# Kernel optimization log

Measured on AMD Instinct MI355X. Metric: run time of the kernel, lower is better.

## Reference

```python
import jax, jax.numpy as jnp
from jax import lax
import numpy as np

KERNEL = 3
DILATION = 2
STRIDE = 2
MU = 0.1


def mask_dial(kernel_size, dilation, mu):
    # Faithful numpy port of CustomConv.mask_dial (constant fuzzy mask).
    d = dilation - 1
    mid = [0.0] * d
    lim = d // 2 if d % 2 == 0 else d // 2 + 1
    diff = (1.0 - mu) / lim
    for i in range(lim):
        mid[i] = 1.0 - (i + 1) * diff
        mid[d - 1 - i] = 1.0 - (i + 1) * diff
    filter1 = []
    for i in range(2 * kernel_size - 1):
        filter1 = filter1 + ([0.0] if i % 2 == 0 else mid)
    filter2 = [[0.0 for _ in range(d + 2)] for _ in range(d)]
    for i in range(lim):
        for j in range(i + 2):
            filter2[i][j] = mid[i]
            filter2[i][d + 1 - j] = mid[i]
            filter2[d - i - 1][j] = mid[i]
            filter2[d - i - 1][d + 1 - j] = mid[i]
        for j in range(i + 1, lim):
            filter2[i][j + 1] = mid[j]
            filter2[i][d - j] = mid[j]
            filter2[d - i - 1][j + 1] = mid[j]
            filter2[d - i - 1][d - j] = mid[j]
    filter3 = [x[1:] for x in filter2]
    for i in range(kernel_size - 2):
        for j in range(len(filter2)):
            filter2[j] = filter2[j] + filter3[j]
    result = []
    for i in range(2 * kernel_size - 1):
        result = result + ([filter1] if i % 2 == 0 else filter2)
    m = np.array(result, dtype=np.float32)
    m[m == 1.0] = 0.0  # self.fuz[self.fuz == 1] = 0
    return m

# constant (kk, kk) mask, kk = dilation*(kernel-1)+1 = 5
FUZ_MASK = jnp.asarray(mask_dial(KERNEL, DILATION, MU))


def setup_inputs() -> dict:
    key = jax.random.key(0)
    k1, k2, k3 = jax.random.split(key, 3)
    B, Cin, H, W = 16, 128, 112, 112
    Cout = 256
    stdv = float(np.sqrt(6.0 / (Cin * KERNEL ** 2 + Cout * KERNEL ** 2)))
    input_ = jax.random.normal(k1, (B, Cin, H, W), dtype=jnp.float32)
    weight = jax.random.uniform(k2, (Cout, Cin, KERNEL, KERNEL), minval=-stdv, maxval=stdv, dtype=jnp.float32)
    bias1 = jax.random.uniform(k3, (Cout,), minval=-stdv, maxval=stdv, dtype=jnp.float32)
    return {"input_": input_, "weight": weight, "bias1": bias1}


def reference(input_, weight, bias1):
    Cout, Cin = weight.shape[0], weight.shape[1]
    dn = ("NCHW", "OIHW", "NCHW")
    # term 1: standard dilated conv (im2col with kernel=3, dilation=2 in original)
    out_w = lax.conv_general_dilated(
        input_, weight, window_strides=(STRIDE, STRIDE), padding="VALID",
        rhs_dilation=(DILATION, DILATION), dimension_numbers=dn)
    # term 2: fuzzy conv: kernel = fuz_mask * bias1[o], dense 5x5, dilation 1
    kk = FUZ_MASK.shape[0]
    fuz_kernel = bias1[:, None, None, None] * jnp.broadcast_to(
        FUZ_MASK.astype(input_.dtype), (Cout, Cin, kk, kk))
    out_f = lax.conv_general_dilated(
        input_, fuz_kernel, window_strides=(STRIDE, STRIDE), padding="VALID",
        dimension_numbers=dn)
    return out_w + out_f
```

## Files before the change

kernel.cpp:

```cpp
#include <hip/hip_runtime.h>
#include <hip/hip_bf16.h>

typedef __bf16 bf16x8 __attribute__((ext_vector_type(8)));
typedef float f32x4 __attribute__((ext_vector_type(4)));
typedef unsigned short u16x8 __attribute__((ext_vector_type(8)));

#define B_    16
#define CIN   128
#define H_    112
#define W_    112
#define COUT  256
#define HO    54
#define WO    54
#define M_PER_B (HO*WO)
#define HW    (H_*W_)

__device__ __forceinline__ unsigned short f2bf(float v) {
    __hip_bfloat16 h = __float2bfloat16(v);
    return __builtin_bit_cast(unsigned short, h);
}

__global__ __launch_bounds__(256) void sum_kernel(
    const float* __restrict__ in, const float* __restrict__ w,
    float* __restrict__ S, unsigned short* __restrict__ Wf)
{
    const int blk = blockIdx.x;
    const int tid = threadIdx.x;
    if (blk < B_ * H_) {
        __shared__ f32x4 red[8][28];
        const int b = blk / H_, h = blk % H_;
        if (tid < 224) {
            const int cg = tid / 28, ws = tid % 28;
            const float* p = in + ((size_t)(b * CIN + cg * 16) * H_ + h) * W_ + 4 * ws;
            f32x4 acc = (f32x4){0.f, 0.f, 0.f, 0.f};
            #pragma unroll
            for (int k = 0; k < 16; ++k)
                acc += *reinterpret_cast<const f32x4*>(p + (size_t)k * HW);
            red[cg][ws] = acc;
        }
        __syncthreads();
        if (tid < 28) {
            f32x4 s = red[0][tid];
            #pragma unroll
            for (int g = 1; g < 8; ++g) s += red[g][tid];
            *reinterpret_cast<f32x4*>(S + (size_t)(b * H_ + h) * W_ + 4 * tid) = s;
        }
    } else {
        int cid = (blk - B_ * H_) * 256 + tid;
        if (cid < 9 * 4 * 16 * 64) {
            int L   = cid & 63;
            int g   = (cid >> 6) & 15;
            int c0  = (cid >> 10) & 3;
            int t   = cid >> 12;
            int o   = g * 16 + (L & 15);
            int cb  = c0 * 32 + (L >> 4) * 8;
            u16x8 v;
            #pragma unroll
            for (int e = 0; e < 8; ++e)
                v[e] = f2bf(w[(size_t)(o * CIN + cb + e) * 9 + t]);
            *reinterpret_cast<u16x8*>(Wf + (size_t)cid * 8) = v;
        }
    }
}

__global__ __launch_bounds__(128) void t_kernel(
    const float* __restrict__ S, float* __restrict__ T)
{
    __shared__ float Sr[5][112];
    const int blk = blockIdx.x;
    const int tid = threadIdx.x;
    const int b = blk / HO, y = blk % HO;
    for (int task = tid; task < 5 * 28; task += 128) {
        int row = task / 28, w4 = task % 28;
        *reinterpret_cast<f32x4*>(&Sr[row][4 * w4]) =
            *reinterpret_cast<const f32x4*>(S + (size_t)(b * H_ + 2 * y + row) * W_ + 4 * w4);
    }
    __syncthreads();
    if (tid < WO) {
        int x = tid;
        float s25 = 0.f, s9 = 0.f;
        #pragma unroll
        for (int i = 0; i < 5; ++i) {
            #pragma unroll
            for (int j = 0; j < 5; ++j) {
                float v = Sr[i][2 * x + j];
                s25 += v;
                if (!(i & 1) && !(j & 1)) s9 += v;
            }
        }
        T[(size_t)b * M_PER_B + y * WO + x] = 0.1f * (s25 - s9);
    }
}

__global__ __launch_bounds__(256, 3) void conv_kernel(
    const float* __restrict__ in, const unsigned short* __restrict__ Wf,
    const float* __restrict__ T, const float* __restrict__ bias1,
    float* __restrict__ out)
{
    __shared__ unsigned short patch[168 * 128];

    const int tid = threadIdx.x;
    int bid = blockIdx.x;
    int wg  = (bid & 7) * 108 + (bid >> 3);
    const int b = wg / HO;
    const int y = wg % HO;

    const float* inb = in + (size_t)b * CIN * HW;
    #pragma unroll
    for (int it = 0; it < 42; ++it) {
        int ch = tid + it * 256;
        int ws = ch % 28;
        int cr = ch / 28;
        int r  = cr % 3;
        int c  = cr / 3;
        f32x4 v = *reinterpret_cast<const f32x4*>(
            inb + ((size_t)c * H_ + (2 * y + 2 * r)) * W_ + 4 * ws);
        int p0 = r * 56 + 2 * ws;
        patch[p0 * 128 + (c ^ ((p0 & 7) << 3))] = f2bf(v[0]);
        int p1 = p0 + 1;
        patch[p1 * 128 + (c ^ ((p1 & 7) << 3))] = f2bf(v[2]);
    }
    __syncthreads();

    const int lane = tid & 63;
    const int wn   = tid >> 6;
    const int lm   = lane & 15;
    const int kq   = lane >> 4;
    const int koff = kq * 8;

    int xm[4];
    #pragma unroll
    for (int mi = 0; mi < 4; ++mi) {
        int x = mi * 16 + lm;
        xm[mi] = (x > 53) ? 53 : x;
    }

    f32x4 acc[4][4];
    #pragma unroll
    for (int mi = 0; mi < 4; ++mi)
        #pragma unroll
        for (int ni = 0; ni < 4; ++ni)
            acc[mi][ni] = (f32x4){0.f, 0.f, 0.f, 0.f};

    const unsigned short* wfl = Wf + (size_t)(wn * 4) * 512 + lane * 8;

    bf16x8 bb[2][4];
    #pragma unroll
    for (int ni = 0; ni < 4; ++ni)
        bb[0][ni] = __builtin_bit_cast(bf16x8,
            *reinterpret_cast<const u16x8*>(wfl + ni * 512));

    #pragma unroll
    for (int s = 0; s < 36; ++s) {
        const int cur = s & 1;
        if (s + 1 < 36) {
            const unsigned short* wnx = wfl + (size_t)(s + 1) * 16 * 512;
            #pragma unroll
            for (int ni = 0; ni < 4; ++ni)
                bb[cur ^ 1][ni] = __builtin_bit_cast(bf16x8,
                    *reinterpret_cast<const u16x8*>(wnx + ni * 512));
        }
        const int t  = s >> 2, c0 = s & 3;
        const int ki = t / 3, kj = t % 3;
        bf16x8 a[4];
        #pragma unroll
        for (int mi = 0; mi < 4; ++mi) {
            int pos = ki * 56 + kj + xm[mi];
            int sa  = pos * 128 + ((c0 * 32 + koff) ^ ((pos & 7) << 3));
            a[mi] = __builtin_bit_cast(bf16x8,
                *reinterpret_cast<const u16x8*>(&patch[sa]));
        }
        #pragma unroll
        for (int mi = 0; mi < 4; ++mi)
            #pragma unroll
            for (int ni = 0; ni < 4; ++ni)
                acc[mi][ni] = __builtin_amdgcn_mfma_f32_16x16x32_bf16(
                    a[mi], bb[cur][ni], acc[mi][ni], 0, 0, 0);
    }

    const float* Trow = T + (size_t)b * M_PER_B + y * WO;
    float* obase = out + (size_t)b * COUT * M_PER_B + y * WO;
    #pragma unroll
    for (int mi = 0; mi < 4; ++mi) {
        int mb = mi * 16 + kq * 4;
        if (mb >= WO) continue;
        bool full = (mb + 4 <= WO);
        float tv0 = Trow[mb], tv1 = Trow[mb + 1];
        float tv2 = 0.f, tv3 = 0.f;
        if (full) { tv2 = Trow[mb + 2]; tv3 = Trow[mb + 3]; }
        #pragma unroll
        for (int ni = 0; ni < 4; ++ni) {
            int o = wn * 64 + ni * 16 + lm;
            float bo = bias1[o];
            float* op = obase + (size_t)o * M_PER_B + mb;
            float2 r01 = make_float2(acc[mi][ni][0] + bo * tv0,
                                     acc[mi][ni][1] + bo * tv1);
            *reinterpret_cast<float2*>(op) = r01;
            if (full) {
                float2 r23 = make_float2(acc[mi][ni][2] + bo * tv2,
                                         acc[mi][ni][3] + bo * tv3);
                *reinterpret_cast<float2*>(op + 2) = r23;
            }
        }
    }
}

extern "C" void kernel_launch(void* const* d_in, const int* in_sizes, int n_in,
                              void* d_out, int out_size, void* d_ws, size_t ws_size,
                              hipStream_t stream)
{
    const float* in = (const float*)d_in[0];
    const float* w  = (const float*)d_in[1];
    const float* b1 = (const float*)d_in[2];
    float* out = (float*)d_out;

    char* ws = (char*)d_ws;
    float* S = (float*)ws;
    size_t off = 802816;
    float* T = (float*)(ws + off);  off += 186624;
    unsigned short* Wf = (unsigned short*)(ws + off);

    sum_kernel<<<dim3(B_ * H_ + 144), 256, 0, stream>>>(in, w, S, Wf);
    t_kernel<<<dim3(B_ * HO), 128, 0, stream>>>(S, T);
    conv_kernel<<<dim3(HO * B_), 256, 0, stream>>>(in, Wf, T, b1, out);
}
```

Baseline: 229.4 us.

## Stage conv input patch in two channel halves to halve LDS footprint

```diff
diff --git a/kernel.cpp b/kernel.cpp
--- a/kernel.cpp
+++ b/kernel.cpp
@@ -92,12 +92,30 @@
     }
 }
 
+#define STAGE_PASS(P)                                                          \
+    {                                                                          \
+        _Pragma("unroll")                                                      \
+        for (int it = 0; it < 21; ++it) {                                      \
+            int id = tid + it * 256;                               \
+            int ws = id % 28;                                                  \
+            int cr = id / 28;                                                  \
+            int r  = cr % 3;                                                   \
+            int c  = cr / 3;                          \
+            f32x4 v = *reinterpret_cast<const f32x4*>(                         \
+                inb + ((size_t)((P) * 64 + c) * H_ + (2 * y + 2 * r)) * W_ + 4 * ws); \
+            int p0 = r * 56 + 2 * ws;                                          \
+            patch[p0 * 64 + (c ^ ((p0 & 7) << 3))] = f2bf(v[0]);               \
+            int p1 = p0 + 1;                                                   \
+            patch[p1 * 64 + (c ^ ((p1 & 7) << 3))] = f2bf(v[2]);               \
+        }                                                                      \
+    }
+
 __global__ __launch_bounds__(256, 3) void conv_kernel(
     const float* __restrict__ in, const unsigned short* __restrict__ Wf,
     const float* __restrict__ T, const float* __restrict__ bias1,
     float* __restrict__ out)
 {
-    __shared__ unsigned short patch[168 * 128];
+    __shared__ unsigned short patch[168 * 64];
 
     const int tid = threadIdx.x;
     int bid = blockIdx.x;
@@ -106,27 +124,13 @@
     const int y = wg % HO;
 
     const float* inb = in + (size_t)b * CIN * HW;
-    #pragma unroll
-    for (int it = 0; it < 42; ++it) {
-        int ch = tid + it * 256;
-        int ws = ch % 28;
-        int cr = ch / 28;
-        int r  = cr % 3;
-        int c  = cr / 3;
-        f32x4 v = *reinterpret_cast<const f32x4*>(
-            inb + ((size_t)c * H_ + (2 * y + 2 * r)) * W_ + 4 * ws);
-        int p0 = r * 56 + 2 * ws;
-        patch[p0 * 128 + (c ^ ((p0 & 7) << 3))] = f2bf(v[0]);
-        int p1 = p0 + 1;
-        patch[p1 * 128 + (c ^ ((p1 & 7) << 3))] = f2bf(v[2]);
-    }
+    STAGE_PASS(0)
     __syncthreads();
 
     const int lane = tid & 63;
     const int wn   = tid >> 6;
     const int lm   = lane & 15;
     const int kq   = lane >> 4;
-    const int koff = kq * 8;
 
     int xm[4];
     #pragma unroll
@@ -153,20 +157,30 @@
     #pragma unroll
     for (int s = 0; s < 36; ++s) {
         const int cur = s & 1;
+        if (s == 18) {
+            __syncthreads();
+            STAGE_PASS(1)
+            __syncthreads();
+        }
         if (s + 1 < 36) {
-            const unsigned short* wnx = wfl + (size_t)(s + 1) * 16 * 512;
+            const int sn = s + 1;
+            const int pn = sn / 18, rn = sn % 18;
+            const int slab_n = (rn >> 1) * 4 + 2 * pn + (rn & 1);
+            const unsigned short* wnx = wfl + (size_t)slab_n * 16 * 512;
             #pragma unroll
             for (int ni = 0; ni < 4; ++ni)
                 bb[cur ^ 1][ni] = __builtin_bit_cast(bf16x8,
                     *reinterpret_cast<const u16x8*>(wnx + ni * 512));
         }
-        const int t  = s >> 2, c0 = s & 3;
+        const int rr = s % 18;
+        const int t  = rr >> 1;
         const int ki = t / 3, kj = t % 3;
+        const int coff = (rr & 1) * 32 + kq * 8;
         bf16x8 a[4];
         #pragma unroll
         for (int mi = 0; mi < 4; ++mi) {
             int pos = ki * 56 + kj + xm[mi];
-            int sa  = pos * 128 + ((c0 * 32 + koff) ^ ((pos & 7) << 3));
+            int sa  = pos * 64 + (coff ^ ((pos & 7) << 3));
             a[mi] = __builtin_bit_cast(bf16x8,
                 *reinterpret_cast<const u16x8*>(&patch[sa]));
         }
```

Result: slower. 269.1 us (+17.3%).
